# Kernel optimization log

Hardware: AMD Instinct MI355X
Metric: run time of the kernel (lower is better)

Reference implementation:

```python
import jax, jax.numpy as jnp
import numpy as np

B, IN, N, W, R, U, OUT = 512, 128, 256, 64, 4, 256, 128
IFACE = R * W + 3 * W + 5 * R + 3  # 471
CLIP = 20.0
EPS = 1e-6


def setup_inputs() -> dict:
    key = jax.random.key(0)
    ks = jax.random.split(key, 20)
    return {
        'inputs': jax.random.normal(ks[0], (B, IN), jnp.float32),
        'M': jax.random.normal(ks[1], (B, N, W), jnp.float32),
        'usage': jax.random.uniform(ks[2], (B, N), jnp.float32),
        'link': jax.random.uniform(ks[3], (B, N, N), jnp.float32) * 0.01,
        'precedence': jax.random.uniform(ks[4], (B, N), jnp.float32) * 0.01,
        'ww_prev': jax.random.uniform(ks[5], (B, N), jnp.float32) / N,
        'wr_prev': jax.random.uniform(ks[6], (B, N, R), jnp.float32) / N,
        'h_prev': jax.random.normal(ks[7], (B, U), jnp.float32),
        'c_prev': jax.random.normal(ks[8], (B, U), jnp.float32),
        'rv_prev': jax.random.normal(ks[9], (B, W, R), jnp.float32),
        'Wk': jax.random.normal(ks[10], (IN + W * R, 4 * U), jnp.float32) * 0.05,
        'Wr': jax.random.normal(ks[11], (U, 4 * U), jnp.float32) * 0.05,
        'b_lstm': jnp.full((4 * U,), 0.1, jnp.float32),
        'Wi': jax.random.normal(ks[12], (U, IFACE), jnp.float32) * 0.05,
        'bi': jnp.full((IFACE,), 0.1, jnp.float32),
        'Wo': jax.random.normal(ks[13], (U + W * R, OUT), jnp.float32) * 0.05,
        'bo': jnp.zeros((OUT,), jnp.float32),
    }


def _parse_interface(v):
    sizes = [R * W, R, W, 1, W, W, R, 1, 1, 3 * R]
    offs = np.cumsum([0] + sizes)
    s = [v[:, offs[i]:offs[i + 1]] for i in range(len(sizes))]
    read_keys = s[0].reshape(-1, W, R)
    read_strengths = 1.0 + jax.nn.softplus(s[1])                 # [B,R]
    write_key = s[2].reshape(-1, W)                              # [B,W]
    write_strength = 1.0 + jax.nn.softplus(s[3])                 # [B,1]
    erase = jax.nn.sigmoid(s[4])                                 # [B,W]
    write_vec = s[5]                                             # [B,W]
    free_gates = jax.nn.sigmoid(s[6])                            # [B,R]
    alloc_gate = jax.nn.sigmoid(s[7])                            # [B,1]
    write_gate = jax.nn.sigmoid(s[8])                            # [B,1]
    read_modes = jax.nn.softmax(s[9].reshape(-1, 3, R), axis=1)  # [B,3,R]
    return (read_keys, read_strengths, write_key, write_strength, erase,
            write_vec, free_gates, alloc_gate, write_gate, read_modes)


def _forward(inputs, M, usage, link, precedence, ww_prev, wr_prev,
             h_prev, c_prev, rv_prev, Wk, Wr, b_lstm, Wi, bi, Wo, bo):
    # --- controller (keras LSTMCell: gate order i,f,c,o) ---
    x = jnp.concatenate([inputs, rv_prev.reshape(-1, W * R)], axis=1)
    z = x @ Wk + h_prev @ Wr + b_lstm
    zi, zf, zc, zo = jnp.split(z, 4, axis=1)
    c = jax.nn.sigmoid(zf) * c_prev + jax.nn.sigmoid(zi) * jnp.tanh(zc)
    h = jax.nn.sigmoid(zo) * jnp.tanh(c)
    h = jnp.clip(h, -CLIP, CLIP)
    # --- interface ---
    (read_keys, read_strengths, write_key, write_strength, erase,
     write_vec, free_gates, alloc_gate, write_gate, read_modes) = _parse_interface(h @ Wi + bi)
    # --- usage / retention ---
    psi = jnp.prod(1.0 - free_gates[:, None, :] * wr_prev, axis=2)     # [B,N]
    u = (usage + ww_prev - usage * ww_prev) * psi                      # [B,N]
    # --- allocation (sorted cumprod) ---
    idx = jnp.argsort(u, axis=1)                                        # ascending
    u_sorted = jnp.take_along_axis(u, idx, axis=1)
    cp = jnp.cumprod(u_sorted, axis=1)
    cp_excl = jnp.concatenate([jnp.ones_like(cp[:, :1]), cp[:, :-1]], axis=1)
    a_sorted = (1.0 - u_sorted) * cp_excl
    inv = jnp.argsort(idx, axis=1)
    alloc = jnp.take_along_axis(a_sorted, inv, axis=1)                  # [B,N]
    # --- write content addressing (cosine) ---
    Mn = jnp.linalg.norm(M, axis=2)                                     # [B,N]
    kw_n = jnp.linalg.norm(write_key, axis=1, keepdims=True)            # [B,1]
    sim_w = jnp.einsum('bnw,bw->bn', M, write_key) / (Mn * kw_n + EPS)
    cw = jax.nn.softmax(write_strength * sim_w, axis=1)                 # [B,N]
    ww = write_gate * (alloc_gate * alloc + (1.0 - alloc_gate) * cw)    # [B,N]
    # --- memory write ---
    M_new = M * (1.0 - ww[:, :, None] * erase[:, None, :]) + ww[:, :, None] * write_vec[:, None, :]
    # --- temporal link / precedence ---
    L_new = (1.0 - ww[:, :, None] - ww[:, None, :]) * link + ww[:, :, None] * precedence[:, None, :]
    L_new = L_new * (1.0 - jnp.eye(N, dtype=L_new.dtype))
    p_new = (1.0 - jnp.sum(ww, axis=1, keepdims=True)) * precedence + ww
    # --- read content addressing ---
    Mn2 = jnp.linalg.norm(M_new, axis=2)                                # [B,N]
    kr_n = jnp.linalg.norm(read_keys, axis=1)                           # [B,R]
    sim_r = jnp.einsum('bnw,bwr->bnr', M_new, read_keys) / (Mn2[:, :, None] * kr_n[:, None, :] + EPS)
    cr = jax.nn.softmax(read_strengths[:, None, :] * sim_r, axis=1)     # [B,N,R]
    # --- forward / backward weightings ---
    fwd = jnp.einsum('bnm,bmr->bnr', L_new, wr_prev)
    bwd = jnp.einsum('bmn,bmr->bnr', L_new, wr_prev)
    wr = (read_modes[:, 0, :][:, None, :] * bwd
          + read_modes[:, 1, :][:, None, :] * cr
          + read_modes[:, 2, :][:, None, :] * fwd)                      # [B,N,R]
    read_vectors = jnp.einsum('bnw,bnr->bwr', M_new, wr)                # [B,W,R]
    # --- final output ---
    final = jnp.concatenate([h, read_vectors.reshape(-1, W * R)], axis=1) @ Wo + bo
    return jnp.clip(final, -CLIP, CLIP)


def reference(inputs, M, usage, link, precedence, ww_prev, wr_prev,
              h_prev, c_prev, rv_prev, Wk, Wr, b_lstm, Wi, bi, Wo, bo):
    return _forward(inputs, M, usage, link, precedence, ww_prev, wr_prev,
                    h_prev, c_prev, rv_prev, Wk, Wr, b_lstm, Wi, bi, Wo, bo)
```

## Files before the change

### kernel.cpp

```cpp
#include <hip/hip_runtime.h>
#include <math.h>

#define Bsz 512
#define INsz 128
#define Nn 256
#define Ww 64
#define Rr 4
#define Uu 256
#define OUTsz 128
#define IFACEsz 471
#define XDIM 384
#define KL 640
#define G4 1024

__device__ __forceinline__ float sigf(float x){ return 1.0f/(1.0f+expf(-x)); }
__device__ __forceinline__ float softplusf_(float x){ return fmaxf(x,0.0f) + log1pf(expf(-fabsf(x))); }
__device__ __forceinline__ float4 f4fma(float s, float4 a, float4 acc){
  acc.x += s*a.x; acc.y += s*a.y; acc.z += s*a.z; acc.w += s*a.w; return acc;
}
__device__ __forceinline__ float4 f4add(float4 a, float4 b){
  a.x+=b.x; a.y+=b.y; a.z+=b.z; a.w+=b.w; return a;
}
__device__ __forceinline__ float4 f4max(float4 a, float4 b){
  a.x=fmaxf(a.x,b.x); a.y=fmaxf(a.y,b.y); a.z=fmaxf(a.z,b.z); a.w=fmaxf(a.w,b.w); return a;
}

__global__ __launch_bounds__(256) void k_packWi(
  const float* __restrict__ Wi, float* __restrict__ Wip)
{
  const int k = blockIdx.x, t = threadIdx.x;
  const int j2 = t + 256;
  Wip[(size_t)k*512 + t]  = Wi[(size_t)k*IFACEsz + t];
  Wip[(size_t)k*512 + j2] = (j2 < IFACEsz) ? Wi[(size_t)k*IFACEsz + j2] : 0.0f;
}

__global__ __launch_bounds__(512) void k_lstm(
  const float* __restrict__ inputs, const float* __restrict__ rvp,
  const float* __restrict__ hp, const float* __restrict__ Wk,
  const float* __restrict__ Wr, const float* __restrict__ bl,
  const float* __restrict__ cprev, float* __restrict__ h_out)
{
  const int t = threadIdx.x;
  const int tx = t & 7;
  const int tg = (t >> 3) & 3;
  const int tb = t >> 5;
  const int b0 = blockIdx.x * 16;
  const int cg = blockIdx.y * 32;
  const int col = tg*256 + cg + tx*4;
  __shared__ float Xs[16][68];
  __shared__ float zs[16][4][36];
  float4 acc = {0,0,0,0};
  for (int kc = 0; kc < KL; kc += 64){
    if (t < 256){
      const int rr = t >> 4, cc = (t & 15)*4;
      const int c = kc + cc;
      const float* src;
      if (c < INsz)      src = inputs + (size_t)(b0+rr)*INsz + c;
      else if (c < XDIM) src = rvp + (size_t)(b0+rr)*(Ww*Rr) + (c - INsz);
      else               src = hp + (size_t)(b0+rr)*Uu + (c - XDIM);
      *reinterpret_cast<float4*>(&Xs[rr][cc]) = *reinterpret_cast<const float4*>(src);
    }
    __syncthreads();
    const float* Wp = ((kc < XDIM) ? (Wk + (size_t)kc*G4) : (Wr + (size_t)(kc-XDIM)*G4)) + col;
    #pragma unroll 8
    for (int kk=0; kk<64; ++kk){
      float4 w4 = *reinterpret_cast<const float4*>(Wp + (size_t)kk*G4);
      acc = f4fma(Xs[tb][kk], w4, acc);
    }
    __syncthreads();
  }
  {
    float4 b4 = *reinterpret_cast<const float4*>(bl + col);
    acc = f4add(acc, b4);
  }
  *reinterpret_cast<float4*>(&zs[tb][tg][tx*4]) = acc;
  __syncthreads();
  {
    const int b = t >> 5, c = t & 31;
    float zi = zs[b][0][c], zf = zs[b][1][c], zc_ = zs[b][2][c], zo = zs[b][3][c];
    float cc = sigf(zf)*cprev[(size_t)(b0+b)*Uu + cg + c] + sigf(zi)*tanhf(zc_);
    float h = sigf(zo)*tanhf(cc);
    h = fminf(fmaxf(h,-20.0f),20.0f);
    h_out[(size_t)(b0+b)*Uu + cg + c] = h;
  }
}

__global__ __launch_bounds__(256) void k_ifgemm(
  const float* __restrict__ h_ws, const float* __restrict__ Wip, float* __restrict__ v_ws)
{
  const int t = threadIdx.x;
  const int tx = t & 15, ty = t >> 4;
  const int b0 = blockIdx.x*16;
  const int col = blockIdx.y*64 + tx*4;
  __shared__ float Hs[16][68];
  float4 acc = {0,0,0,0};
  for (int kc = 0; kc < Uu; kc += 64){
    {
      int rr = t >> 4, cc = (t & 15)*4;
      *reinterpret_cast<float4*>(&Hs[rr][cc]) =
        *reinterpret_cast<const float4*>(h_ws + (size_t)(b0+rr)*Uu + kc + cc);
    }
    __syncthreads();
    const float* Wp = Wip + (size_t)kc*512 + col;
    #pragma unroll 8
    for (int kk=0; kk<64; ++kk){
      float4 w4 = *reinterpret_cast<const float4*>(Wp + (size_t)kk*512);
      acc = f4fma(Hs[ty][kk], w4, acc);
    }
    __syncthreads();
  }
  *reinterpret_cast<float4*>(v_ws + (size_t)(b0+ty)*512 + col) = acc;
}

__global__ __launch_bounds__(256) void k_iface2(
  const float* __restrict__ v_ws, const float* __restrict__ bi,
  const float* __restrict__ usage, const float* __restrict__ wwp,
  const float* __restrict__ wrp, const float* __restrict__ prec,
  const float* __restrict__ M,
  float* __restrict__ ww_ws, float* __restrict__ er_ws, float* __restrict__ wv_ws,
  float* __restrict__ rk_ws, float* __restrict__ krn_ws, float* __restrict__ rstr_ws,
  float* __restrict__ rm_ws, float* __restrict__ P_ws, float* __restrict__ Q_ws)
{
  const int b = blockIdx.x, t = threadIdx.x;
  __shared__ float vl[IFACEsz];
  __shared__ float wkey[Ww];
  __shared__ float ul[Nn], sul[Nn], cpl[Nn], red[Nn];
  __shared__ __align__(16) float4 red4[Nn];
  __shared__ float scal[8];
  for (int j=t; j<IFACEsz; j+=256) vl[j] = v_ws[(size_t)b*512 + j] + bi[j];
  __syncthreads();
  if (t < Ww){
    wkey[t] = vl[260+t];
    er_ws[b*Ww+t] = sigf(vl[325+t]);
    wv_ws[b*Ww+t] = vl[389+t];
  }
  rk_ws[b*Ww*Rr + t] = vl[t];
  if (t < Rr){
    rstr_ws[b*Rr+t] = 1.0f + softplusf_(vl[256+t]);
    float ssum = 0.0f;
    for (int w=0;w<Ww;++w){ float v = vl[w*Rr+t]; ssum += v*v; }
    krn_ws[b*Rr+t] = sqrtf(ssum);
    float q0=vl[459+t], q1=vl[463+t], q2=vl[467+t];
    float mm = fmaxf(q0, fmaxf(q1,q2));
    float e0=expf(q0-mm), e1=expf(q1-mm), e2=expf(q2-mm);
    float inv = 1.0f/(e0+e1+e2);
    rm_ws[b*12 + t]     = e0*inv;
    rm_ws[b*12 + 4 + t] = e1*inv;
    rm_ws[b*12 + 8 + t] = e2*inv;
    scal[4+t] = sigf(vl[453+t]);
  }
  if (t == 0){
    scal[0] = 1.0f + softplusf_(vl[324]);
    scal[1] = sigf(vl[457]);
    scal[2] = sigf(vl[458]);
    float ssum=0.0f;
    for (int w=0;w<Ww;++w){ float v=vl[260+w]; ssum += v*v; }
    scal[3] = sqrtf(ssum);
  }
  __syncthreads();
  float4 wr4 = *reinterpret_cast<const float4*>(wrp + ((size_t)b*Nn + t)*Rr);
  float psi = (1.0f - scal[4]*wr4.x)*(1.0f - scal[5]*wr4.y)
            * (1.0f - scal[6]*wr4.z)*(1.0f - scal[7]*wr4.w);
  float us = usage[b*Nn+t], wp = wwp[b*Nn+t];
  float u = (us + wp - us*wp)*psi;
  ul[t] = u;
  __syncthreads();
  int rank = 0;
  for (int m=0;m<Nn;++m){
    float um = ul[m];
    rank += (um < u || (um == u && m < t)) ? 1 : 0;
  }
  sul[rank] = u;
  __syncthreads();
  cpl[t] = sul[t];
  __syncthreads();
  for (int d=1; d<Nn; d<<=1){
    float a = cpl[t];
    float m_ = (t >= d) ? cpl[t-d] : 1.0f;
    __syncthreads();
    cpl[t] = a*m_;
    __syncthreads();
  }
  float cpexcl = (rank == 0) ? 1.0f : cpl[rank-1];
  float alloc = (1.0f - u)*cpexcl;
  const float* Mrow = M + ((size_t)b*Nn + t)*Ww;
  float dot=0.0f, nrm=0.0f;
  #pragma unroll 4
  for (int w=0;w<Ww;w+=4){
    float4 m4 = *reinterpret_cast<const float4*>(Mrow + w);
    dot += m4.x*wkey[w] + m4.y*wkey[w+1] + m4.z*wkey[w+2] + m4.w*wkey[w+3];
    nrm += m4.x*m4.x + m4.y*m4.y + m4.z*m4.z + m4.w*m4.w;
  }
  float sim = dot/(sqrtf(nrm)*scal[3] + 1e-6f);
  float sc = scal[0]*sim;
  red[t] = sc; __syncthreads();
  for (int st=128; st>0; st>>=1){ if (t<st) red[t] = fmaxf(red[t], red[t+st]); __syncthreads(); }
  float mx = red[0]; __syncthreads();
  float e = expf(sc - mx);
  red[t] = e; __syncthreads();
  for (int st=128; st>0; st>>=1){ if (t<st) red[t] += red[t+st]; __syncthreads(); }
  float cw = e/red[0];
  float ww = scal[2]*(scal[1]*alloc + (1.0f - scal[1])*cw);
  ww_ws[b*Nn+t] = ww;
  __syncthreads();
  float pr = prec[b*Nn+t];
  float4 pv; pv.x = pr*wr4.x; pv.y = pr*wr4.y; pv.z = pr*wr4.z; pv.w = pr*wr4.w;
  red4[t] = pv; __syncthreads();
  for (int st=128; st>0; st>>=1){ if (t<st) red4[t] = f4add(red4[t], red4[t+st]); __syncthreads(); }
  if (t==0) *reinterpret_cast<float4*>(P_ws + b*Rr) = red4[0];
  __syncthreads();
  float4 qv; qv.x = ww*wr4.x; qv.y = ww*wr4.y; qv.z = ww*wr4.z; qv.w = ww*wr4.w;
  red4[t] = qv; __syncthreads();
  for (int st=128; st>0; st>>=1){ if (t<st) red4[t] = f4add(red4[t], red4[t+st]); __syncthreads(); }
  if (t==0) *reinterpret_cast<float4*>(Q_ws + b*Rr) = red4[0];
}

__global__ __launch_bounds__(256) void k_link(
  const float* __restrict__ link, const float* __restrict__ wrp,
  const float* __restrict__ ww_ws,
  float* __restrict__ rowA, float* __restrict__ rowC,
  float* __restrict__ colAp, float* __restrict__ colCp, float* __restrict__ diag)
{
  const int b = blockIdx.x, s = blockIdx.y, t = threadIdx.x;
  const int n0 = s*64;
  __shared__ __align__(16) float4 wrl4[Nn];
  __shared__ __align__(16) float4 wrl4p[4][66];
  __shared__ float wws[Nn];
  __shared__ float wwsp[4][68];
  __shared__ __align__(16) float4 cred[4][Nn];
  {
    float4 w4 = *reinterpret_cast<const float4*>(wrp + ((size_t)b*Nn + t)*Rr);
    wrl4[t] = w4;
    wrl4p[t>>6][t&63] = w4;
    float w = ww_ws[(size_t)b*Nn + t];
    wws[t] = w;
    wwsp[t>>6][t&63] = w;
  }
  __syncthreads();
  const float* Lb = link + (size_t)b*Nn*Nn;
  const int cq = t & 63, g = t >> 6;
  const int c4 = cq*4;
  {
    float4 z = {0,0,0,0};
    float4 a0=z,a1=z,a2=z,a3=z, q0=z,q1=z,q2=z,q3=z;
    #pragma unroll
    for (int i=0;i<16;++i){
      const int n = n0 + g*16 + i;
      float4 l4 = *reinterpret_cast<const float4*>(Lb + (size_t)n*Nn + c4);
      float4 wn = wrl4[n];
      float wwn = wws[n];
      a0 = f4fma(l4.x, wn, a0); a1 = f4fma(l4.y, wn, a1);
      a2 = f4fma(l4.z, wn, a2); a3 = f4fma(l4.w, wn, a3);
      q0 = f4fma(l4.x*wwn, wn, q0); q1 = f4fma(l4.y*wwn, wn, q1);
      q2 = f4fma(l4.z*wwn, wn, q2); q3 = f4fma(l4.w*wwn, wn, q3);
      if ((n>>2) == cq){
        const int r = n&3;
        float c = (r==0) ? l4.x : (r==1) ? l4.y : (r==2) ? l4.z : l4.w;
        diag[(size_t)b*Nn + n] = c;
      }
    }
    cred[g][c4+0]=a0; cred[g][c4+1]=a1; cred[g][c4+2]=a2; cred[g][c4+3]=a3;
    __syncthreads();
    {
      float4 sA = f4add(f4add(cred[0][t],cred[1][t]),f4add(cred[2][t],cred[3][t]));
      *reinterpret_cast<float4*>(colAp + (((size_t)s*Bsz + b)*Nn + t)*Rr) = sA;
    }
    __syncthreads();
    cred[g][c4+0]=q0; cred[g][c4+1]=q1; cred[g][c4+2]=q2; cred[g][c4+3]=q3;
    __syncthreads();
    {
      float4 sC = f4add(f4add(cred[0][t],cred[1][t]),f4add(cred[2][t],cred[3][t]));
      *reinterpret_cast<float4*>(colCp + (((size_t)s*Bsz + b)*Nn + t)*Rr) = sC;
    }
  }
  {
    const int row = n0 + (t >> 2), seg = t & 3;
    const float* Lr = Lb + (size_t)row*Nn + seg*64;
    float ra0=0,ra1=0,ra2=0,ra3=0, rc0=0,rc1=0,rc2=0,rc3=0;
    #pragma unroll
    for (int k=0;k<16;++k){
      float4 l4 = *reinterpret_cast<const float4*>(Lr + k*4);
      float4 ww4 = *reinterpret_cast<const float4*>(&wwsp[seg][k*4]);
      float4 w0 = wrl4p[seg][k*4], w1 = wrl4p[seg][k*4+1];
      float4 w2 = wrl4p[seg][k*4+2], w3 = wrl4p[seg][k*4+3];
      ra0 += l4.x*w0.x + l4.y*w1.x + l4.z*w2.x + l4.w*w3.x;
      ra1 += l4.x*w0.y + l4.y*w1.y + l4.z*w2.y + l4.w*w3.y;
      ra2 += l4.x*w0.z + l4.y*w1.z + l4.z*w2.z + l4.w*w3.z;
      ra3 += l4.x*w0.w + l4.y*w1.w + l4.z*w2.w + l4.w*w3.w;
      float lx=l4.x*ww4.x, ly=l4.y*ww4.y, lz=l4.z*ww4.z, lw=l4.w*ww4.w;
      rc0 += lx*w0.x + ly*w1.x + lz*w2.x + lw*w3.x;
      rc1 += lx*w0.y + ly*w1.y + lz*w2.y + lw*w3.y;
      rc2 += lx*w0.z + ly*w1.z + lz*w2.z + lw*w3.z;
      rc3 += lx*w0.w + ly*w1.w + lz*w2.w + lw*w3.w;
    }
    #pragma unroll
    for (int off=2; off>=1; off>>=1){
      ra0 += __shfl_down(ra0, off, 4); ra1 += __shfl_down(ra1, off, 4);
      ra2 += __shfl_down(ra2, off, 4); ra3 += __shfl_down(ra3, off, 4);
      rc0 += __shfl_down(rc0, off, 4); rc1 += __shfl_down(rc1, off, 4);
      rc2 += __shfl_down(rc2, off, 4); rc3 += __shfl_down(rc3, off, 4);
    }
    if (seg == 0){
      float4 oA; oA.x=ra0; oA.y=ra1; oA.z=ra2; oA.w=ra3;
      float4 oC; oC.x=rc0; oC.y=rc1; oC.z=rc2; oC.w=rc3;
      *reinterpret_cast<float4*>(rowA + ((size_t)b*Nn + row)*Rr) = oA;
      *reinterpret_cast<float4*>(rowC + ((size_t)b*Nn + row)*Rr) = oC;
    }
  }
}

__global__ __launch_bounds__(256) void k_readw_rv(
  const float* __restrict__ M, const float* __restrict__ ww_ws,
  const float* __restrict__ er_ws, const float* __restrict__ wv_ws,
  const float* __restrict__ rk_ws, const float* __restrict__ krn_ws,
  const float* __restrict__ rstr_ws, const float* __restrict__ rm_ws,
  const float* __restrict__ P_ws, const float* __restrict__ Q_ws,
  const float* __restrict__ rowA, const float* __restrict__ rowC,
  const float* __restrict__ colAp, const float* __restrict__ colCp,
  const float* __restrict__ diag, const float* __restrict__ wrp,
  const float* __restrict__ prec, float* __restrict__ rv_ws)
{
  const int b = blockIdx.x, t = threadIdx.x;
  __shared__ float rkl[Ww*Rr];
  __shared__ float erl[Ww], wvl[Ww];
  __shared__ __align__(16) float4 red4[Nn];
  __shared__ float wrl[Nn][4];
  __shared__ float wwl[Nn];
  rkl[t] = rk_ws[b*Ww*Rr + t];
  if (t < Ww){ erl[t] = er_ws[b*Ww+t]; wvl[t] = wv_ws[b*Ww+t]; }
  const float ww = ww_ws[b*Nn+t];
  wwl[t] = ww;
  __syncthreads();
  const float pr = prec[b*Nn+t];
  const float dg = diag[b*Nn+t];
  float4 wr4 = *reinterpret_cast<const float4*>(wrp + ((size_t)b*Nn+t)*Rr);
  const float Lnn = (1.0f - 2.0f*ww)*dg + ww*pr;
  float4 rA = *reinterpret_cast<const float4*>(rowA + ((size_t)b*Nn+t)*Rr);
  float4 rC = *reinterpret_cast<const float4*>(rowC + ((size_t)b*Nn+t)*Rr);
  float4 cA = {0,0,0,0}, cC = {0,0,0,0};
  #pragma unroll
  for (int sp=0; sp<4; ++sp){
    cA = f4add(cA, *reinterpret_cast<const float4*>(colAp + (((size_t)sp*Bsz + b)*Nn + t)*Rr));
    cC = f4add(cC, *reinterpret_cast<const float4*>(colCp + (((size_t)sp*Bsz + b)*Nn + t)*Rr));
  }
  float4 Pv = *reinterpret_cast<const float4*>(P_ws + b*Rr);
  float4 Qv = *reinterpret_cast<const float4*>(Q_ws + b*Rr);
  float fwdv[4], bwdv[4];
  fwdv[0] = (1.0f-ww)*rA.x - rC.x + ww*Pv.x - Lnn*wr4.x;
  fwdv[1] = (1.0f-ww)*rA.y - rC.y + ww*Pv.y - Lnn*wr4.y;
  fwdv[2] = (1.0f-ww)*rA.z - rC.z + ww*Pv.z - Lnn*wr4.z;
  fwdv[3] = (1.0f-ww)*rA.w - rC.w + ww*Pv.w - Lnn*wr4.w;
  bwdv[0] = (1.0f-ww)*cA.x - cC.x + pr*Qv.x - Lnn*wr4.x;
  bwdv[1] = (1.0f-ww)*cA.y - cC.y + pr*Qv.y - Lnn*wr4.y;
  bwdv[2] = (1.0f-ww)*cA.z - cC.z + pr*Qv.z - Lnn*wr4.z;
  bwdv[3] = (1.0f-ww)*cA.w - cC.w + pr*Qv.w - Lnn*wr4.w;
  const float* Mrow = M + ((size_t)b*Nn + t)*Ww;
  float s0=0,s1=0,s2=0,s3=0, nrm=0;
  #pragma unroll 4
  for (int w=0;w<Ww;w+=4){
    float4 m4 = *reinterpret_cast<const float4*>(Mrow + w);
    float mvs[4] = {m4.x, m4.y, m4.z, m4.w};
    #pragma unroll
    for (int i=0;i<4;++i){
      int w_ = w+i;
      float mn = mvs[i]*(1.0f - ww*erl[w_]) + ww*wvl[w_];
      nrm += mn*mn;
      float4 k4 = *reinterpret_cast<const float4*>(&rkl[w_*4]);
      s0 += mn*k4.x; s1 += mn*k4.y; s2 += mn*k4.z; s3 += mn*k4.w;
    }
  }
  float mnorm = sqrtf(nrm);
  float4 kn = *reinterpret_cast<const float4*>(krn_ws + b*Rr);
  float4 rs = *reinterpret_cast<const float4*>(rstr_ws + b*Rr);
  float4 aa4;
  aa4.x = rs.x*(s0/(mnorm*kn.x + 1e-6f));
  aa4.y = rs.y*(s1/(mnorm*kn.y + 1e-6f));
  aa4.z = rs.z*(s2/(mnorm*kn.z + 1e-6f));
  aa4.w = rs.w*(s3/(mnorm*kn.w + 1e-6f));
  red4[t] = aa4; __syncthreads();
  for (int st=128; st>0; st>>=1){ if (t<st) red4[t] = f4max(red4[t], red4[t+st]); __syncthreads(); }
  float4 mx4 = red4[0]; __syncthreads();
  float4 e4;
  e4.x = expf(aa4.x - mx4.x); e4.y = expf(aa4.y - mx4.y);
  e4.z = expf(aa4.z - mx4.z); e4.w = expf(aa4.w - mx4.w);
  red4[t] = e4; __syncthreads();
  for (int st=128; st>0; st>>=1){ if (t<st) red4[t] = f4add(red4[t], red4[t+st]); __syncthreads(); }
  float4 sm4 = red4[0];
  float cr[4] = {e4.x/sm4.x, e4.y/sm4.y, e4.z/sm4.z, e4.w/sm4.w};
  float wro[4];
  #pragma unroll
  for (int r=0;r<4;++r){
    float m0 = rm_ws[b*12 + r];
    float m1 = rm_ws[b*12 + 4 + r];
    float m2 = rm_ws[b*12 + 8 + r];
    wro[r] = m0*bwdv[r] + m1*cr[r] + m2*fwdv[r];
  }
  wrl[t][0]=wro[0]; wrl[t][1]=wro[1]; wrl[t][2]=wro[2]; wrl[t][3]=wro[3];
  __syncthreads();
  {
    const int w = t & 63, r = t >> 6;
    const float er_w = erl[w], wv_w = wvl[w];
    float a0=0.0f, a1=0.0f, a2=0.0f, a3=0.0f;
    for (int n=0;n<Nn;n+=4){
      float m0v = M[((size_t)b*Nn + n  )*Ww + w];
      float m1v = M[((size_t)b*Nn + n+1)*Ww + w];
      float m2v = M[((size_t)b*Nn + n+2)*Ww + w];
      float m3v = M[((size_t)b*Nn + n+3)*Ww + w];
      float w0 = wwl[n], w1 = wwl[n+1], w2 = wwl[n+2], w3 = wwl[n+3];
      a0 += (m0v*(1.0f - w0*er_w) + w0*wv_w)*wrl[n  ][r];
      a1 += (m1v*(1.0f - w1*er_w) + w1*wv_w)*wrl[n+1][r];
      a2 += (m2v*(1.0f - w2*er_w) + w2*wv_w)*wrl[n+2][r];
      a3 += (m3v*(1.0f - w3*er_w) + w3*wv_w)*wrl[n+3][r];
    }
    rv_ws[(size_t)b*(Ww*Rr) + w*Rr + r] = (a0+a1)+(a2+a3);
  }
}

__global__ __launch_bounds__(256) void k_final(
  const float* __restrict__ h_ws, const float* __restrict__ rv_ws,
  const float* __restrict__ Wo, const float* __restrict__ bo,
  float* __restrict__ out)
{
  const int t = threadIdx.x;
  const int tx = t & 15, ty = t >> 4;
  const int b0 = blockIdx.x*16;
  const int col = blockIdx.y*64 + tx*4;
  __shared__ float Cs[16][68];
  float4 acc = {0,0,0,0};
  for (int kc = 0; kc < 512; kc += 64){
    {
      int rr = t >> 4, cc = (t & 15)*4;
      const float* src = (kc < Uu)
        ? (h_ws  + (size_t)(b0+rr)*Uu + kc + cc)
        : (rv_ws + (size_t)(b0+rr)*(Ww*Rr) + (kc-Uu) + cc);
      *reinterpret_cast<float4*>(&Cs[rr][cc]) = *reinterpret_cast<const float4*>(src);
    }
    __syncthreads();
    const float* Wp = Wo + (size_t)kc*OUTsz + col;
    #pragma unroll 8
    for (int kk=0; kk<64; ++kk){
      float4 w4 = *reinterpret_cast<const float4*>(Wp + (size_t)kk*OUTsz);
      acc = f4fma(Cs[ty][kk], w4, acc);
    }
    __syncthreads();
  }
  float4 b4 = *reinterpret_cast<const float4*>(bo + col);
  acc.x = fminf(fmaxf(acc.x + b4.x, -20.0f), 20.0f);
  acc.y = fminf(fmaxf(acc.y + b4.y, -20.0f), 20.0f);
  acc.z = fminf(fmaxf(acc.z + b4.z, -20.0f), 20.0f);
  acc.w = fminf(fmaxf(acc.w + b4.w, -20.0f), 20.0f);
  *reinterpret_cast<float4*>(out + (size_t)(b0+ty)*OUTsz + col) = acc;
}

extern "C" void kernel_launch(void* const* d_in, const int* in_sizes, int n_in,
                              void* d_out, int out_size, void* d_ws, size_t ws_size,
                              hipStream_t stream)
{
  const float* inputs = (const float*)d_in[0];
  const float* M      = (const float*)d_in[1];
  const float* usage  = (const float*)d_in[2];
  const float* link   = (const float*)d_in[3];
  const float* prec   = (const float*)d_in[4];
  const float* wwp    = (const float*)d_in[5];
  const float* wrp    = (const float*)d_in[6];
  const float* hp     = (const float*)d_in[7];
  const float* cp     = (const float*)d_in[8];
  const float* rvp    = (const float*)d_in[9];
  const float* Wk     = (const float*)d_in[10];
  const float* Wr     = (const float*)d_in[11];
  const float* bl     = (const float*)d_in[12];
  const float* Wi     = (const float*)d_in[13];
  const float* bi     = (const float*)d_in[14];
  const float* Wo     = (const float*)d_in[15];
  const float* bo     = (const float*)d_in[16];

  float* ws = (float*)d_ws;
  float* Wip     = ws;
  float* v_ws    = Wip    + (size_t)Uu*512;
  float* h_ws    = v_ws   + (size_t)Bsz*512;
  float* ww_ws   = h_ws   + (size_t)Bsz*Uu;
  float* er_ws   = ww_ws  + (size_t)Bsz*Nn;
  float* wv_ws   = er_ws  + (size_t)Bsz*Ww;
  float* rk_ws   = wv_ws  + (size_t)Bsz*Ww;
  float* krn_ws  = rk_ws  + (size_t)Bsz*Ww*Rr;
  float* rstr_ws = krn_ws + (size_t)Bsz*Rr;
  float* rm_ws   = rstr_ws+ (size_t)Bsz*Rr;
  float* P_ws    = rm_ws  + (size_t)Bsz*3*Rr;
  float* Q_ws    = P_ws   + (size_t)Bsz*Rr;
  float* rowA    = Q_ws   + (size_t)Bsz*Rr;
  float* rowC    = rowA   + (size_t)Bsz*Nn*Rr;
  float* colAp   = rowC   + (size_t)Bsz*Nn*Rr;
  float* colCp   = colAp  + (size_t)4*Bsz*Nn*Rr;
  float* diag    = colCp  + (size_t)4*Bsz*Nn*Rr;
  float* rv_ws   = diag   + (size_t)Bsz*Nn;

  k_packWi<<<dim3(Uu), dim3(256), 0, stream>>>(Wi, Wip);
  k_lstm<<<dim3(32,8), dim3(512), 0, stream>>>(inputs, rvp, hp, Wk, Wr, bl, cp, h_ws);
  k_ifgemm<<<dim3(32,8), dim3(256), 0, stream>>>(h_ws, Wip, v_ws);
  k_iface2<<<dim3(Bsz), dim3(256), 0, stream>>>(v_ws, bi, usage, wwp, wrp, prec, M,
      ww_ws, er_ws, wv_ws, rk_ws, krn_ws, rstr_ws, rm_ws, P_ws, Q_ws);
  k_link<<<dim3(Bsz,4), dim3(256), 0, stream>>>(link, wrp, ww_ws, rowA, rowC, colAp, colCp, diag);
  k_readw_rv<<<dim3(Bsz), dim3(256), 0, stream>>>(M, ww_ws, er_ws, wv_ws, rk_ws, krn_ws,
      rstr_ws, rm_ws, P_ws, Q_ws, rowA, rowC, colAp, colCp, diag, wrp, prec, rv_ws);
  k_final<<<dim3(32,2), dim3(256), 0, stream>>>(h_ws, rv_ws, Wo, bo, (float*)d_out);
}
```

Baseline: 188.9 us.

## Fuse row and column link reductions into a single pass over link

The link kernel previously read each 64-row slab of the link matrix twice: once for column-wise products and once for row-wise products. It now computes both from the same loaded float4, keeping per-thread weight fragments in registers and reducing row sums across the wavefront with xor shuffles. This removes the duplicate global read and the padded shared arrays. In exchange it adds many cross-lane shuffles per row.

Result: slower. 217.3 us (+15.0%).

```diff
diff --git a/kernel.cpp b/kernel.cpp
--- a/kernel.cpp
+++ b/kernel.cpp
@@ -24,6 +24,7 @@
 __device__ __forceinline__ float4 f4max(float4 a, float4 b){
   a.x=fmaxf(a.x,b.x); a.y=fmaxf(a.y,b.y); a.z=fmaxf(a.z,b.z); a.w=fmaxf(a.w,b.w); return a;
 }
+__device__ __forceinline__ float4 L4(const float* p){ return *reinterpret_cast<const float4*>(p); }
 
 __global__ __launch_bounds__(256) void k_packWi(
   const float* __restrict__ Wi, float* __restrict__ Wip)
@@ -224,88 +225,75 @@
   const int b = blockIdx.x, s = blockIdx.y, t = threadIdx.x;
   const int n0 = s*64;
   __shared__ __align__(16) float4 wrl4[Nn];
-  __shared__ __align__(16) float4 wrl4p[4][66];
   __shared__ float wws[Nn];
-  __shared__ float wwsp[4][68];
   __shared__ __align__(16) float4 cred[4][Nn];
   {
-    float4 w4 = *reinterpret_cast<const float4*>(wrp + ((size_t)b*Nn + t)*Rr);
-    wrl4[t] = w4;
-    wrl4p[t>>6][t&63] = w4;
-    float w = ww_ws[(size_t)b*Nn + t];
-    wws[t] = w;
-    wwsp[t>>6][t&63] = w;
-  }
-  __syncthreads();
-  const float* Lb = link + (size_t)b*Nn*Nn;
+    wrl4[t] = L4(wrp + ((size_t)b*Nn + t)*Rr);
+    wws[t]  = ww_ws[(size_t)b*Nn + t];
+  }
+  __syncthreads();
   const int cq = t & 63, g = t >> 6;
   const int c4 = cq*4;
-  {
-    float4 z = {0,0,0,0};
-    float4 a0=z,a1=z,a2=z,a3=z, q0=z,q1=z,q2=z,q3=z;
-    #pragma unroll
-    for (int i=0;i<16;++i){
-      const int n = n0 + g*16 + i;
-      float4 l4 = *reinterpret_cast<const float4*>(Lb + (size_t)n*Nn + c4);
+  const float4 w0 = wrl4[c4], w1 = wrl4[c4+1], w2 = wrl4[c4+2], w3 = wrl4[c4+3];
+  float4 ww4; ww4.x = wws[c4]; ww4.y = wws[c4+1]; ww4.z = wws[c4+2]; ww4.w = wws[c4+3];
+  const float* Lb = link + (size_t)b*Nn*Nn;
+  float4 z = {0,0,0,0};
+  float4 cA0=z,cA1=z,cA2=z,cA3=z, cC0=z,cC1=z,cC2=z,cC3=z;
+  #pragma unroll 4
+  for (int i=0;i<16;++i){
+    const int n = n0 + g*16 + i;
+    float4 l4 = L4(Lb + (size_t)n*Nn + c4);
+    if ((n>>2) == cq){
+      const int r = n & 3;
+      float d = (r==0)?l4.x : (r==1)?l4.y : (r==2)?l4.z : l4.w;
+      diag[(size_t)b*Nn + n] = d;
+    }
+    {
       float4 wn = wrl4[n];
       float wwn = wws[n];
-      a0 = f4fma(l4.x, wn, a0); a1 = f4fma(l4.y, wn, a1);
-      a2 = f4fma(l4.z, wn, a2); a3 = f4fma(l4.w, wn, a3);
-      q0 = f4fma(l4.x*wwn, wn, q0); q1 = f4fma(l4.y*wwn, wn, q1);
-      q2 = f4fma(l4.z*wwn, wn, q2); q3 = f4fma(l4.w*wwn, wn, q3);
-      if ((n>>2) == cq){
-        const int r = n&3;
-        float c = (r==0) ? l4.x : (r==1) ? l4.y : (r==2) ? l4.z : l4.w;
-        diag[(size_t)b*Nn + n] = c;
+      float4 wnw; wnw.x=wwn*wn.x; wnw.y=wwn*wn.y; wnw.z=wwn*wn.z; wnw.w=wwn*wn.w;
+      cA0 = f4fma(l4.x, wn, cA0); cA1 = f4fma(l4.y, wn, cA1);
+      cA2 = f4fma(l4.z, wn, cA2); cA3 = f4fma(l4.w, wn, cA3);
+      cC0 = f4fma(l4.x, wnw, cC0); cC1 = f4fma(l4.y, wnw, cC1);
+      cC2 = f4fma(l4.z, wnw, cC2); cC3 = f4fma(l4.w, wnw, cC3);
+    }
+    {
+      float pa0 = l4.x*w0.x + l4.y*w1.x + l4.z*w2.x + l4.w*w3.x;
+      float pa1 = l4.x*w0.y + l4.y*w1.y + l4.z*w2.y + l4.w*w3.y;
+      float pa2 = l4.x*w0.z + l4.y*w1.z + l4.z*w2.z + l4.w*w3.z;
+      float pa3 = l4.x*w0.w + l4.y*w1.w + l4.z*w2.w + l4.w*w3.w;
+      float lx=l4.x*ww4.x, ly=l4.y*ww4.y, lz=l4.z*ww4.z, lw=l4.w*ww4.w;
+      float pc0 = lx*w0.x + ly*w1.x + lz*w2.x + lw*w3.x;
+      float pc1 = lx*w0.y + ly*w1.y + lz*w2.y + lw*w3.y;
+      float pc2 = lx*w0.z + ly*w1.z + lz*w2.z + lw*w3.z;
+      float pc3 = lx*w0.w + ly*w1.w + lz*w2.w + lw*w3.w;
+      #pragma unroll
+      for (int m=1; m<64; m<<=1){
+        pa0 += __shfl_xor(pa0, m); pa1 += __shfl_xor(pa1, m);
+        pa2 += __shfl_xor(pa2, m); pa3 += __shfl_xor(pa3, m);
+        pc0 += __shfl_xor(pc0, m); pc1 += __shfl_xor(pc1, m);
+        pc2 += __shfl_xor(pc2, m); pc3 += __shfl_xor(pc3, m);
       }
-    }
-    cred[g][c4+0]=a0; cred[g][c4+1]=a1; cred[g][c4+2]=a2; cred[g][c4+3]=a3;
-    __syncthreads();
-    {
-      float4 sA = f4add(f4add(cred[0][t],cred[1][t]),f4add(cred[2][t],cred[3][t]));
-      *reinterpret_cast<float4*>(colAp + (((size_t)s*Bsz + b)*Nn + t)*Rr) = sA;
-    }
-    __syncthreads();
-    cred[g][c4+0]=q0; cred[g][c4+1]=q1; cred[g][c4+2]=q2; cred[g][c4+3]=q3;
-    __syncthreads();
-    {
-      float4 sC = f4add(f4add(cred[0][t],cred[1][t]),f4add(cred[2][t],cred[3][t]));
-      *reinterpret_cast<float4*>(colCp + (((size_t)s*Bsz + b)*Nn + t)*Rr) = sC;
-    }
-  }
-  {
-    const int row = n0 + (t >> 2), seg = t & 3;
-    const float* Lr = Lb + (size_t)row*Nn + seg*64;
-    float ra0=0,ra1=0,ra2=0,ra3=0, rc0=0,rc1=0,rc2=0,rc3=0;
-    #pragma unroll
-    for (int k=0;k<16;++k){
-      float4 l4 = *reinterpret_cast<const float4*>(Lr + k*4);
-      float4 ww4 = *reinterpret_cast<const float4*>(&wwsp[seg][k*4]);
-      float4 w0 = wrl4p[seg][k*4], w1 = wrl4p[seg][k*4+1];
-      float4 w2 = wrl4p[seg][k*4+2], w3 = wrl4p[seg][k*4+3];
-      ra0 += l4.x*w0.x + l4.y*w1.x + l4.z*w2.x + l4.w*w3.x;
-      ra1 += l4.x*w0.y + l4.y*w1.y + l4.z*w2.y + l4.w*w3.y;
-      ra2 += l4.x*w0.z + l4.y*w1.z + l4.z*w2.z + l4.w*w3.z;
-      ra3 += l4.x*w0.w + l4.y*w1.w + l4.z*w2.w + l4.w*w3.w;
-      float lx=l4.x*ww4.x, ly=l4.y*ww4.y, lz=l4.z*ww4.z, lw=l4.w*ww4.w;
-      rc0 += lx*w0.x + ly*w1.x + lz*w2.x + lw*w3.x;
-      rc1 += lx*w0.y + ly*w1.y + lz*w2.y + lw*w3.y;
-      rc2 += lx*w0.z + ly*w1.z + lz*w2.z + lw*w3.z;
-      rc3 += lx*w0.w + ly*w1.w + lz*w2.w + lw*w3.w;
-    }
-    #pragma unroll
-    for (int off=2; off>=1; off>>=1){
-      ra0 += __shfl_down(ra0, off, 4); ra1 += __shfl_down(ra1, off, 4);
-      ra2 += __shfl_down(ra2, off, 4); ra3 += __shfl_down(ra3, off, 4);
-      rc0 += __shfl_down(rc0, off, 4); rc1 += __shfl_down(rc1, off, 4);
-      rc2 += __shfl_down(rc2, off, 4); rc3 += __shfl_down(rc3, off, 4);
-    }
-    if (seg == 0){
-      float4 oA; oA.x=ra0; oA.y=ra1; oA.z=ra2; oA.w=ra3;
-      float4 oC; oC.x=rc0; oC.y=rc1; oC.z=rc2; oC.w=rc3;
-      *reinterpret_cast<float4*>(rowA + ((size_t)b*Nn + row)*Rr) = oA;
-      *reinterpret_cast<float4*>(rowC + ((size_t)b*Nn + row)*Rr) = oC;
-    }
+      if (cq == 0){
+        float4 oA; oA.x=pa0; oA.y=pa1; oA.z=pa2; oA.w=pa3;
+        float4 oC; oC.x=pc0; oC.y=pc1; oC.z=pc2; oC.w=pc3;
+        *reinterpret_cast<float4*>(rowA + ((size_t)b*Nn + n)*Rr) = oA;
+        *reinterpret_cast<float4*>(rowC + ((size_t)b*Nn + n)*Rr) = oC;
+      }
+    }
+  }
+  cred[g][c4+0]=cA0; cred[g][c4+1]=cA1; cred[g][c4+2]=cA2; cred[g][c4+3]=cA3;
+  __syncthreads();
+  {
+    float4 sA = f4add(f4add(cred[0][t],cred[1][t]),f4add(cred[2][t],cred[3][t]));
+    *reinterpret_cast<float4*>(colAp + (((size_t)s*Bsz + b)*Nn + t)*Rr) = sA;
+  }
+  __syncthreads();
+  cred[g][c4+0]=cC0; cred[g][c4+1]=cC1; cred[g][c4+2]=cC2; cred[g][c4+3]=cC3;
+  __syncthreads();
+  {
+    float4 sC = f4add(f4add(cred[0][t],cred[1][t]),f4add(cred[2][t],cred[3][t]));
+    *reinterpret_cast<float4*>(colCp + (((size_t)s*Bsz + b)*Nn + t)*Rr) = sC;
   }
 }
 
```
